# Kernel tuning notes

Hardware: AMD Instinct MI355X
Metric: run time of the kernel (lower is better)

The kernel has to match this reference:

```python
import jax, jax.numpy as jnp
import numpy as np

B, N, K, E = 2, 131072, 20, 256  # batch, points, n_slot, feat/embed dim
GN_GROUPS = 4
IOU_THR = 0.5
SCORE_THR = 0.04
TEMP = 0.05


def setup_inputs() -> dict:
    key = jax.random.key(0)
    ks = jax.random.split(key, 6)
    wscale = 1.0 / np.sqrt(E)
    return {
        "features": jax.random.normal(ks[0], (B, N, E), jnp.float32),
        "slots": jax.random.normal(ks[1], (B, K, E), jnp.float32),
        "w1": jax.random.normal(ks[2], (E, E), jnp.float32) * wscale,
        "b1": jax.random.normal(ks[3], (E,), jnp.float32) * 0.01,
        "gn_g": jnp.ones((E,), jnp.float32),
        "gn_b": jnp.zeros((E,), jnp.float32),
        "w2": jax.random.normal(ks[4], (E, E), jnp.float32) * wscale,
        "b2": jax.random.normal(ks[5], (E,), jnp.float32) * 0.01,
    }


def _l2norm(x, axis):
    n = jnp.linalg.norm(x, axis=axis, keepdims=True)
    return x / jnp.maximum(n, 1e-12)  # F.normalize semantics


def _nms_filter(mask):
    # mask: [N, K] soft instance probabilities (rows sum to 1)
    scores = mask.mean(axis=0)                       # [K]
    valid = scores >= SCORE_THR
    order = jnp.argsort(-scores)                     # descending score
    sm = mask[:, order]                              # [N, K] sorted columns
    bm = (sm > 0.5).astype(mask.dtype).T             # [K, N] binary masks
    areas = bm.sum(axis=1)                           # [K]
    inter = bm @ bm.T                                # [K, K] pairwise intersections
    union = areas[:, None] + areas[None, :] - inter
    iou = inter / (union + 1e-8)
    idx = jnp.arange(K)
    sup0 = ~valid[order]                             # invalid slots pre-suppressed

    def body(i, sup):
        keep_i = ~sup[i]
        return sup | (keep_i & (iou[i] > IOU_THR) & (idx > i))

    sup = jax.lax.fori_loop(0, K, body, sup0)
    kept = ~sup                                      # [K]
    # kept columns are packed (in score order) into the left of the output;
    # dropped columns are routed to a dump column K which is sliced away.
    pos = jnp.cumsum(kept) - 1
    cols = jnp.where(kept, pos, K)
    out = jnp.zeros((mask.shape[0], K + 1), mask.dtype).at[:, cols].set(sm)
    out = out[:, :K]
    # per-point renormalization over kept masks (zeros stay zero if none kept)
    return out / (out.sum(axis=1, keepdims=True) + 1e-8)


def reference(features, slots, w1, b1, gn_g, gn_b, w2, b2):
    # object_mlp: Conv1d(1x1) -> GroupNorm(4) -> ReLU -> Conv1d(1x1)
    x = jnp.einsum('bke,oe->bok', slots, w1) + b1[None, :, None]   # [B, E, K]
    xg = x.reshape(B, GN_GROUPS, E // GN_GROUPS, K)
    mu = xg.mean(axis=(2, 3), keepdims=True)
    var = xg.var(axis=(2, 3), keepdims=True)
    xg = (xg - mu) * jax.lax.rsqrt(var + 1e-5)
    x = xg.reshape(B, E, K) * gn_g[None, :, None] + gn_b[None, :, None]
    x = jax.nn.relu(x)
    slot = jnp.einsum('bek,fe->bfk', x, w2) + b2[None, :, None]    # [B, F=E, K]

    fn = _l2norm(features, axis=-1)                                # [B, N, E]
    sn = _l2norm(slot, axis=1)                                     # [B, E, K]
    logits = jnp.einsum('bnd,bdk->bnk', fn, sn) / TEMP
    mask = jax.nn.softmax(logits, axis=-1)                         # [B, N, K]

    out = jax.vmap(_nms_filter)(mask)                              # [B, N, K]
    return out.transpose(0, 2, 1)                                  # [B, K, N]
```

## Files before the change

kernel.cpp:

```cpp
#include <hip/hip_runtime.h>

#define B_ 2
#define N_ 131072
#define K_ 20
#define E_ 256
#define TEMP_ 0.05f
#define SCORE_THR_ 0.04f

#define WS_SCORE 0
#define WS_XN    1024
#define WS_SN    16384
#define WS_MASK  32768
#define WS_SPART 6291456

typedef __attribute__((ext_vector_type(8))) short short8;
typedef __attribute__((ext_vector_type(4))) float f32x4;

__device__ inline float wave_sum(float v) {
    #pragma unroll
    for (int off = 32; off; off >>= 1) v += __shfl_xor(v, off, 64);
    return v;
}

__device__ inline void dma16(const void* g, void* l) {
    __builtin_amdgcn_global_load_lds(
        (const __attribute__((address_space(1))) void*)g,
        (__attribute__((address_space(3))) void*)l, 16, 0, 0);
}

__device__ inline void cvt_hilo(const float4 a, const float4 b, short8& h, short8& l) {
    float f[8] = {a.x, a.y, a.z, a.w, b.x, b.y, b.z, b.w};
    #pragma unroll
    for (int j = 0; j < 8; ++j) {
        const unsigned u  = __float_as_uint(f[j]);
        const unsigned hb = (u + 0x7fffu + ((u >> 16) & 1u)) & 0xffff0000u;
        h[j] = (short)(hb >> 16);
        const float r = f[j] - __uint_as_float(hb);
        const unsigned v = __float_as_uint(r);
        l[j] = (short)((v + 0x7fffu + ((v >> 16) & 1u)) >> 16);
    }
}

__global__ __launch_bounds__(256) void kA1(const float* __restrict__ slots,
                                           const float* __restrict__ w1,
                                           const float* __restrict__ b1,
                                           const float* __restrict__ gn_g,
                                           const float* __restrict__ gn_b,
                                           float* __restrict__ ws) {
    __shared__ __align__(16) float slds[20 * 260];
    __shared__ float red[2];
    const int t = threadIdx.x;
    const int b = blockIdx.x >> 2, g = blockIdx.x & 3;
    if (t < 2) red[t] = 0.f;
    const float* sb = slots + (size_t)b * K_ * E_;
    #pragma unroll
    for (int i = 0; i < 20; ++i) slds[i * 260 + t] = sb[i * 256 + t];
    __syncthreads();

    const int c = t >> 2, q = t & 3;
    const int o = g * 64 + c;
    const float* w1r = w1 + (size_t)o * E_;
    float acc[5] = {0.f, 0.f, 0.f, 0.f, 0.f};
    for (int e4 = 0; e4 < 64; ++e4) {
        const float4 w4 = *(const float4*)(w1r + e4 * 4);
        #pragma unroll
        for (int kk = 0; kk < 5; ++kk) {
            const float4 s4 = *(const float4*)&slds[(q * 5 + kk) * 260 + e4 * 4];
            acc[kk] += w4.x * s4.x + w4.y * s4.y + w4.z * s4.z + w4.w * s4.w;
        }
    }
    const float bias = b1[o];
    float s1 = 0.f, s2 = 0.f;
    #pragma unroll
    for (int kk = 0; kk < 5; ++kk) {
        acc[kk] += bias;
        s1 += acc[kk];
        s2 += acc[kk] * acc[kk];
    }
    s1 = wave_sum(s1);
    s2 = wave_sum(s2);
    if ((t & 63) == 0) { atomicAdd(&red[0], s1); atomicAdd(&red[1], s2); }
    __syncthreads();
    const float mean = red[0] * (1.f / 1280.f);
    const float var  = red[1] * (1.f / 1280.f) - mean * mean;
    const float rstd = rsqrtf(var + 1e-5f);
    const float gg = gn_g[o], gb = gn_b[o];
    float* xn = ws + WS_XN + (size_t)b * K_ * E_;
    #pragma unroll
    for (int kk = 0; kk < 5; ++kk) {
        float v = (acc[kk] - mean) * rstd * gg + gb;
        v = v > 0.f ? v : 0.f;
        xn[(q * 5 + kk) * 256 + o] = v;
    }
}

__global__ __launch_bounds__(256) void kA2(const float* __restrict__ w2,
                                           const float* __restrict__ b2,
                                           float* __restrict__ ws) {
    __shared__ __align__(16) float xv[256];
    __shared__ float wred[4];
    const int t = threadIdx.x;
    const int b = blockIdx.x / 20, k = blockIdx.x % 20;
    const float* xn = ws + WS_XN + (size_t)(b * 20 + k) * 256;
    xv[t] = xn[t];
    __syncthreads();
    const float* w2r = w2 + (size_t)t * 256;
    float acc = 0.f;
    for (int e4 = 0; e4 < 64; ++e4) {
        const float4 w4 = *(const float4*)(w2r + e4 * 4);
        const float4 x4 = *(const float4*)&xv[e4 * 4];
        acc += w4.x * x4.x + w4.y * x4.y + w4.z * x4.z + w4.w * x4.w;
    }
    acc += b2[t];
    float sq = wave_sum(acc * acc);
    if ((t & 63) == 0) wred[t >> 6] = sq;
    __syncthreads();
    const float nsq = wred[0] + wred[1] + wred[2] + wred[3];
    const float inv = 1.f / fmaxf(sqrtf(nsq), 1e-12f);
    ws[WS_SN + (size_t)(b * 20 + k) * 256 + t] = acc * inv;
}

__global__ __launch_bounds__(256, 2) void kB(const float* __restrict__ feat,
                                             float* __restrict__ ws) {
    __shared__ short8 sfh[2][8][64];
    __shared__ short8 sfl[2][8][64];
    __shared__ __align__(16) float4 fbuf[4][2][256];
    __shared__ float wsum[4][20];
    const int t = threadIdx.x;
    const int lane = t & 63, w = t >> 6;
    const int b = blockIdx.x >> 9, blk = blockIdx.x & 511;
    const int s = lane & 15, g = lane >> 4;

    {
        #pragma unroll
        for (int i = 0; i < 4; ++i) {
            const int combo = w * 4 + i;
            const int tile = combo >> 3, ks = combo & 7;
            const int slot = tile * 16 + s;
            short8 h, l;
            if (slot < K_) {
                const float* snp = ws + WS_SN + ((size_t)(b * K_ + slot)) * E_
                                 + ks * 32 + g * 8;
                cvt_hilo(*(const float4*)snp, *(const float4*)(snp + 4), h, l);
            } else {
                #pragma unroll
                for (int j = 0; j < 8; ++j) { h[j] = 0; l[j] = 0; }
            }
            sfh[tile][ks][lane] = h;
            sfl[tile][ks][lane] = l;
        }
    }
    __syncthreads();

    const int pA = lane >> 3;
    const int pB = 8 + (lane >> 3);
    const int loff0 = pA * 1024 + ((((lane & 7) - pA) & 7) << 4);
    const int loff1 = pB * 1024 + ((((lane & 7) - pB) & 7) << 4);
    const int loff2 = loff0 + 128;
    const int loff3 = loff1 + 128;
    const char* wbase = (const char*)(feat + ((size_t)b * N_ + (size_t)blk * 256 + w * 64) * E_);

    auto issueQ = [&](int qq) {
        const char* tb = wbase + (qq >> 2) * 16384 + (qq & 3) * 256;
        float4* db = &fbuf[w][qq & 1][0];
        dma16(tb + loff0, db);
        dma16(tb + loff1, db + 64);
        dma16(tb + loff2, db + 128);
        dma16(tb + loff3, db + 192);
    };

    const int ub = ((s >> 3) << 6) + ((s & 7) << 3);
    const int u00 = ub + ((2 * g + 0 + s) & 7);
    const int u01 = ub + ((2 * g + 1 + s) & 7);
    const int u10 = u00 + 128;
    const int u11 = u01 + 128;

    issueQ(0);
    issueQ(1);

    float sreg0 = 0.f, sreg1 = 0.f;

    for (int it = 0; it < 4; ++it) {
        const int pb = w * 64 + it * 16;
        f32x4 c0 = {0.f, 0.f, 0.f, 0.f};
        f32x4 c1 = {0.f, 0.f, 0.f, 0.f};
        float nr = 0.f;
        #pragma unroll
        for (int qi = 0; qi < 4; ++qi) {
            const int q = it * 4 + qi;
            if (q < 15) { asm volatile("s_waitcnt vmcnt(4)" ::: "memory"); }
            else        { asm volatile("s_waitcnt vmcnt(0)" ::: "memory"); }
            __builtin_amdgcn_sched_barrier(0);
            const float4* bq = &fbuf[w][q & 1][0];
            const float4 a0 = bq[u00], b0 = bq[u01];
            const float4 a1 = bq[u10], b1 = bq[u11];
            asm volatile("s_waitcnt lgkmcnt(0)" ::: "memory");
            __builtin_amdgcn_sched_barrier(0);
            if (q + 2 < 16) issueQ(q + 2);
            {
                nr += a0.x*a0.x + a0.y*a0.y + a0.z*a0.z + a0.w*a0.w
                    + b0.x*b0.x + b0.y*b0.y + b0.z*b0.z + b0.w*b0.w;
                short8 fh, fl;
                cvt_hilo(a0, b0, fh, fl);
                const int ks = qi * 2;
                const short8 sh0 = sfh[0][ks][lane], sl0 = sfl[0][ks][lane];
                const short8 sh1 = sfh[1][ks][lane], sl1 = sfl[1][ks][lane];
                c0 = __builtin_amdgcn_mfma_f32_16x16x32_bf16(fh, sh0, c0, 0, 0, 0);
                c1 = __builtin_amdgcn_mfma_f32_16x16x32_bf16(fh, sh1, c1, 0, 0, 0);
                c0 = __builtin_amdgcn_mfma_f32_16x16x32_bf16(fh, sl0, c0, 0, 0, 0);
                c1 = __builtin_amdgcn_mfma_f32_16x16x32_bf16(fh, sl1, c1, 0, 0, 0);
                c0 = __builtin_amdgcn_mfma_f32_16x16x32_bf16(fl, sh0, c0, 0, 0, 0);
                c1 = __builtin_amdgcn_mfma_f32_16x16x32_bf16(fl, sh1, c1, 0, 0, 0);
            }
            {
                nr += a1.x*a1.x + a1.y*a1.y + a1.z*a1.z + a1.w*a1.w
                    + b1.x*b1.x + b1.y*b1.y + b1.z*b1.z + b1.w*b1.w;
                short8 fh, fl;
                cvt_hilo(a1, b1, fh, fl);
                const int ks = qi * 2 + 1;
                const short8 sh0 = sfh[0][ks][lane], sl0 = sfl[0][ks][lane];
                const short8 sh1 = sfh[1][ks][lane], sl1 = sfl[1][ks][lane];
                c0 = __builtin_amdgcn_mfma_f32_16x16x32_bf16(fh, sh0, c0, 0, 0, 0);
                c1 = __builtin_amdgcn_mfma_f32_16x16x32_bf16(fh, sh1, c1, 0, 0, 0);
                c0 = __builtin_amdgcn_mfma_f32_16x16x32_bf16(fh, sl0, c0, 0, 0, 0);
                c1 = __builtin_amdgcn_mfma_f32_16x16x32_bf16(fh, sl1, c1, 0, 0, 0);
                c0 = __builtin_amdgcn_mfma_f32_16x16x32_bf16(fl, sh0, c0, 0, 0, 0);
                c1 = __builtin_amdgcn_mfma_f32_16x16x32_bf16(fl, sh1, c1, 0, 0, 0);
            }
        }
        nr += __shfl_xor(nr, 16, 64);
        nr += __shfl_xor(nr, 32, 64);
        const float scl = rsqrtf(fmaxf(nr, 1e-24f)) * (1.f / TEMP_);

        float p0[4], p1[4];
        #pragma unroll
        for (int r = 0; r < 4; ++r) {
            const float sr = __shfl(scl, 4 * g + r, 64);
            const float x0 = c0[r] * sr;
            const float x1 = c1[r] * sr;
            float m = (s < 4) ? fmaxf(x0, x1) : x0;
            #pragma unroll
            for (int off = 1; off < 16; off <<= 1) m = fmaxf(m, __shfl_xor(m, off, 64));
            const float e0 = __expf(x0 - m);
            const float e1 = (s < 4) ? __expf(x1 - m) : 0.f;
            float su = e0 + e1;
            #pragma unroll
            for (int off = 1; off < 16; off <<= 1) su += __shfl_xor(su, off, 64);
            const float inv = 1.f / su;
            p0[r] = e0 * inv;
            p1[r] = e1 * inv;
        }
        const int col = blk * 256 + pb + 4 * g;
        float* mrow = ws + WS_MASK + ((size_t)b * K_ + s) * N_ + col;
        *(float4*)mrow = make_float4(p0[0], p0[1], p0[2], p0[3]);
        sreg0 += p0[0] + p0[1] + p0[2] + p0[3];
        if (s < 4) {
            float* mrow1 = ws + WS_MASK + ((size_t)b * K_ + 16 + s) * N_ + col;
            *(float4*)mrow1 = make_float4(p1[0], p1[1], p1[2], p1[3]);
            sreg1 += p1[0] + p1[1] + p1[2] + p1[3];
        }
    }

    sreg0 += __shfl_xor(sreg0, 16, 64);
    sreg0 += __shfl_xor(sreg0, 32, 64);
    sreg1 += __shfl_xor(sreg1, 16, 64);
    sreg1 += __shfl_xor(sreg1, 32, 64);
    if (lane < 16) wsum[w][lane] = sreg0;
    if (lane < 4)  wsum[w][16 + lane] = sreg1;
    __syncthreads();
    if (t < 20)
        ws[WS_SPART + (size_t)blockIdx.x * 20 + t] =
            wsum[0][t] + wsum[1][t] + wsum[2][t] + wsum[3][t];
}

__global__ __launch_bounds__(64) void kC(float* __restrict__ ws) {
    const int l = threadIdx.x;
    const int b = blockIdx.x / 20, k = blockIdx.x % 20;
    const float* sp = ws + WS_SPART;
    float sum = 0.f;
    #pragma unroll
    for (int i = 0; i < 8; ++i)
        sum += sp[(size_t)(b * 512 + l + i * 64) * 20 + k];
    sum = wave_sum(sum);
    if (l == 0) ws[WS_SCORE + blockIdx.x] = sum * (1.f / (float)N_);
}

__global__ __launch_bounds__(256) void kD(const float* __restrict__ ws,
                                          float* __restrict__ out) {
    __shared__ float sc[20];
    __shared__ int rnk[20];
    __shared__ int src[20];
    __shared__ int nk_s;
    const int t = threadIdx.x;
    const int b = blockIdx.x >> 9;
    const int n = (blockIdx.x & 511) * 256 + t;
    if (t < 20) sc[t] = ws[WS_SCORE + b * 20 + t];
    if (t == 0) nk_s = 0;
    __syncthreads();
    if (t < 20) {
        const float mys = sc[t];
        int rank = 0;
        for (int j = 0; j < 20; ++j) {
            const float o = sc[j];
            rank += (o > mys) || (o == mys && j < t);
        }
        rnk[t] = rank;
    }
    __syncthreads();
    if (t < 20 && sc[t] >= SCORE_THR_) {
        int pos = 0;
        for (int j = 0; j < 20; ++j)
            pos += (sc[j] >= SCORE_THR_) && (rnk[j] < rnk[t]);
        src[pos] = t;
        atomicAdd(&nk_s, 1);
    }
    __syncthreads();
    const int nk = nk_s;
    const float* mg = ws + WS_MASK + (size_t)b * 20 * N_;
    float mv[20];
    float den = 1e-8f;
    #pragma unroll
    for (int p = 0; p < 20; ++p) {
        float v = 0.f;
        if (p < nk) v = mg[(size_t)src[p] * N_ + n];
        mv[p] = v;
        den += v;
    }
    const float r = 1.f / den;
    float* og = out + (size_t)b * 20 * N_ + n;
    #pragma unroll
    for (int p = 0; p < 20; ++p) og[(size_t)p * N_] = (p < nk) ? mv[p] * r : 0.f;
}

extern "C" void kernel_launch(void* const* d_in, const int* in_sizes, int n_in,
                              void* d_out, int out_size, void* d_ws, size_t ws_size,
                              hipStream_t stream) {
    const float* feat  = (const float*)d_in[0];
    const float* slots = (const float*)d_in[1];
    const float* w1    = (const float*)d_in[2];
    const float* b1    = (const float*)d_in[3];
    const float* gng   = (const float*)d_in[4];
    const float* gnb   = (const float*)d_in[5];
    const float* w2    = (const float*)d_in[6];
    const float* b2    = (const float*)d_in[7];
    float* ws  = (float*)d_ws;
    float* out = (float*)d_out;

    kA1<<<8,    256, 0, stream>>>(slots, w1, b1, gng, gnb, ws);
    kA2<<<40,   256, 0, stream>>>(w2, b2, ws);
    kB <<<1024, 256, 0, stream>>>(feat, ws);
    kC <<<40,   64,  0, stream>>>(ws);
    kD <<<1024, 256, 0, stream>>>(ws, out);
}
```

Before: 424.5 us.

## Fuse slot MLP kernels and replace score reduction kernel with atomics

Merges the two slot-MLP kernels into one 1024-thread block per batch, so the GroupNorm output stays in LDS instead of going through global workspace. It also drops the separate score-reduction kernel: kB now atomically adds per-block column sums into the score buffer, which the fused MLP kernel zeroes, and kD applies the 1/N scale. This cuts two kernel launches and their dependency gaps. The cost is only 2 blocks for the MLP stage, atomic contention on 40 addresses, and non-deterministic float summation order.

Result: slower. 469.8 us (+10.7%).

```diff
diff --git a/kernel.cpp b/kernel.cpp
--- a/kernel.cpp
+++ b/kernel.cpp
@@ -8,10 +8,8 @@
 #define SCORE_THR_ 0.04f
 
 #define WS_SCORE 0
-#define WS_XN    1024
 #define WS_SN    16384
 #define WS_MASK  32768
-#define WS_SPART 6291456
 
 typedef __attribute__((ext_vector_type(8))) short short8;
 typedef __attribute__((ext_vector_type(4))) float f32x4;
@@ -41,24 +39,32 @@
     }
 }
 
-__global__ __launch_bounds__(256) void kA1(const float* __restrict__ slots,
-                                           const float* __restrict__ w1,
-                                           const float* __restrict__ b1,
-                                           const float* __restrict__ gn_g,
-                                           const float* __restrict__ gn_b,
-                                           float* __restrict__ ws) {
+__global__ __launch_bounds__(1024) void kA12(const float* __restrict__ slots,
+                                             const float* __restrict__ w1,
+                                             const float* __restrict__ b1,
+                                             const float* __restrict__ gn_g,
+                                             const float* __restrict__ gn_b,
+                                             const float* __restrict__ w2,
+                                             const float* __restrict__ b2,
+                                             float* __restrict__ ws) {
     __shared__ __align__(16) float slds[20 * 260];
-    __shared__ float red[2];
+    __shared__ __align__(16) float xlds[20 * 260];
+    __shared__ float red[4][2];
+    __shared__ float nred[20][4];
     const int t = threadIdx.x;
-    const int b = blockIdx.x >> 2, g = blockIdx.x & 3;
-    if (t < 2) red[t] = 0.f;
+    const int b = blockIdx.x;
+    const int o = t & 255, q = t >> 8;
+    const int g = o >> 6;
+    if (t < 20) ws[WS_SCORE + b * 20 + t] = 0.f;
+    if (t < 8) red[t >> 1][t & 1] = 0.f;
     const float* sb = slots + (size_t)b * K_ * E_;
     #pragma unroll
-    for (int i = 0; i < 20; ++i) slds[i * 260 + t] = sb[i * 256 + t];
-    __syncthreads();
-
-    const int c = t >> 2, q = t & 3;
-    const int o = g * 64 + c;
+    for (int i = 0; i < 5; ++i) {
+        const int idx = t + i * 1024;
+        slds[(idx >> 8) * 260 + (idx & 255)] = sb[idx];
+    }
+    __syncthreads();
+
     const float* w1r = w1 + (size_t)o * E_;
     float acc[5] = {0.f, 0.f, 0.f, 0.f, 0.f};
     for (int e4 = 0; e4 < 64; ++e4) {
@@ -79,45 +85,46 @@
     }
     s1 = wave_sum(s1);
     s2 = wave_sum(s2);
-    if ((t & 63) == 0) { atomicAdd(&red[0], s1); atomicAdd(&red[1], s2); }
-    __syncthreads();
-    const float mean = red[0] * (1.f / 1280.f);
-    const float var  = red[1] * (1.f / 1280.f) - mean * mean;
+    if ((t & 63) == 0) { atomicAdd(&red[g][0], s1); atomicAdd(&red[g][1], s2); }
+    __syncthreads();
+    const float mean = red[g][0] * (1.f / 1280.f);
+    const float var  = red[g][1] * (1.f / 1280.f) - mean * mean;
     const float rstd = rsqrtf(var + 1e-5f);
     const float gg = gn_g[o], gb = gn_b[o];
-    float* xn = ws + WS_XN + (size_t)b * K_ * E_;
     #pragma unroll
     for (int kk = 0; kk < 5; ++kk) {
         float v = (acc[kk] - mean) * rstd * gg + gb;
         v = v > 0.f ? v : 0.f;
-        xn[(q * 5 + kk) * 256 + o] = v;
-    }
-}
-
-__global__ __launch_bounds__(256) void kA2(const float* __restrict__ w2,
-                                           const float* __restrict__ b2,
-                                           float* __restrict__ ws) {
-    __shared__ __align__(16) float xv[256];
-    __shared__ float wred[4];
-    const int t = threadIdx.x;
-    const int b = blockIdx.x / 20, k = blockIdx.x % 20;
-    const float* xn = ws + WS_XN + (size_t)(b * 20 + k) * 256;
-    xv[t] = xn[t];
-    __syncthreads();
-    const float* w2r = w2 + (size_t)t * 256;
-    float acc = 0.f;
+        xlds[(q * 5 + kk) * 260 + o] = v;
+    }
+    __syncthreads();
+
+    const float* w2r = w2 + (size_t)o * E_;
+    float acc2[5] = {0.f, 0.f, 0.f, 0.f, 0.f};
     for (int e4 = 0; e4 < 64; ++e4) {
         const float4 w4 = *(const float4*)(w2r + e4 * 4);
-        const float4 x4 = *(const float4*)&xv[e4 * 4];
-        acc += w4.x * x4.x + w4.y * x4.y + w4.z * x4.z + w4.w * x4.w;
-    }
-    acc += b2[t];
-    float sq = wave_sum(acc * acc);
-    if ((t & 63) == 0) wred[t >> 6] = sq;
-    __syncthreads();
-    const float nsq = wred[0] + wred[1] + wred[2] + wred[3];
-    const float inv = 1.f / fmaxf(sqrtf(nsq), 1e-12f);
-    ws[WS_SN + (size_t)(b * 20 + k) * 256 + t] = acc * inv;
+        #pragma unroll
+        for (int kk = 0; kk < 5; ++kk) {
+            const float4 x4 = *(const float4*)&xlds[(q * 5 + kk) * 260 + e4 * 4];
+            acc2[kk] += w4.x * x4.x + w4.y * x4.y + w4.z * x4.z + w4.w * x4.w;
+        }
+    }
+    const float bias2 = b2[o];
+    #pragma unroll
+    for (int kk = 0; kk < 5; ++kk) acc2[kk] += bias2;
+    #pragma unroll
+    for (int kk = 0; kk < 5; ++kk) {
+        const float sq = wave_sum(acc2[kk] * acc2[kk]);
+        if ((t & 63) == 0) nred[q * 5 + kk][g] = sq;
+    }
+    __syncthreads();
+    #pragma unroll
+    for (int kk = 0; kk < 5; ++kk) {
+        const int k = q * 5 + kk;
+        const float nsq = nred[k][0] + nred[k][1] + nred[k][2] + nred[k][3];
+        const float inv = 1.f / fmaxf(sqrtf(nsq), 1e-12f);
+        ws[WS_SN + ((size_t)(b * 20 + k)) * 256 + o] = acc2[kk] * inv;
+    }
 }
 
 __global__ __launch_bounds__(256, 2) void kB(const float* __restrict__ feat,
@@ -269,20 +276,8 @@
     if (lane < 4)  wsum[w][16 + lane] = sreg1;
     __syncthreads();
     if (t < 20)
-        ws[WS_SPART + (size_t)blockIdx.x * 20 + t] =
-            wsum[0][t] + wsum[1][t] + wsum[2][t] + wsum[3][t];
-}
-
-__global__ __launch_bounds__(64) void kC(float* __restrict__ ws) {
-    const int l = threadIdx.x;
-    const int b = blockIdx.x / 20, k = blockIdx.x % 20;
-    const float* sp = ws + WS_SPART;
-    float sum = 0.f;
-    #pragma unroll
-    for (int i = 0; i < 8; ++i)
-        sum += sp[(size_t)(b * 512 + l + i * 64) * 20 + k];
-    sum = wave_sum(sum);
-    if (l == 0) ws[WS_SCORE + blockIdx.x] = sum * (1.f / (float)N_);
+        atomicAdd(&ws[WS_SCORE + b * 20 + t],
+                  wsum[0][t] + wsum[1][t] + wsum[2][t] + wsum[3][t]);
 }
 
 __global__ __launch_bounds__(256) void kD(const float* __restrict__ ws,
@@ -294,7 +289,7 @@
     const int t = threadIdx.x;
     const int b = blockIdx.x >> 9;
     const int n = (blockIdx.x & 511) * 256 + t;
-    if (t < 20) sc[t] = ws[WS_SCORE + b * 20 + t];
+    if (t < 20) sc[t] = ws[WS_SCORE + b * 20 + t] * (1.f / (float)N_);
     if (t == 0) nk_s = 0;
     __syncthreads();
     if (t < 20) {
@@ -346,9 +341,7 @@
     float* ws  = (float*)d_ws;
     float* out = (float*)d_out;
 
-    kA1<<<8,    256, 0, stream>>>(slots, w1, b1, gng, gnb, ws);
-    kA2<<<40,   256, 0, stream>>>(w2, b2, ws);
-    kB <<<1024, 256, 0, stream>>>(feat, ws);
-    kC <<<40,   64,  0, stream>>>(ws);
-    kD <<<1024, 256, 0, stream>>>(ws, out);
-}
+    kA12<<<2,   1024, 0, stream>>>(slots, w1, b1, gng, gnb, w2, b2, ws);
+    kB  <<<1024, 256, 0, stream>>>(feat, ws);
+    kD  <<<1024, 256, 0, stream>>>(ws, out);
+}
```
